# Optimization experiments

Measured on AMD Instinct MI355X. Metric: run time of the kernel, lower is better.

The kernel has to match this reference:

```python
import jax, jax.numpy as jnp
import numpy as np

N = 8192
E = 262144
IN_DIM = 128
OUT_DIM = 16


def _linear_params(key, fan_in, fan_out):
    k1, k2 = jax.random.split(key)
    bound = 1.0 / np.sqrt(fan_in)
    W = jax.random.uniform(k1, (fan_in, fan_out), jnp.float32, -bound, bound)
    b = jax.random.uniform(k2, (fan_out,), jnp.float32, -bound, bound)
    return W, b


def setup_inputs() -> dict:
    key = jax.random.key(0)
    ks = jax.random.split(key, 10)
    x = jax.random.normal(ks[0], (N, IN_DIM), jnp.float32)
    edge_index = jax.random.randint(ks[1], (2, E), 0, N, jnp.int64)
    W1, b1 = _linear_params(ks[2], IN_DIM, 128)
    W2, b2 = _linear_params(ks[3], 128, 256)
    W3, b3 = _linear_params(ks[4], 256, 64)
    Wk, bk = _linear_params(ks[5], 256, 256)
    Wq, bq = _linear_params(ks[6], 256, 256)
    Wr, br = _linear_params(ks[7], IN_DIM, 64)
    Wf, bf = _linear_params(ks[8], 64, OUT_DIM)
    ln_g = jnp.ones((64,), jnp.float32)
    ln_b = jnp.zeros((64,), jnp.float32)
    return dict(x=x, edge_index=edge_index, W1=W1, b1=b1, W2=W2, b2=b2,
                W3=W3, b3=b3, Wk=Wk, bk=bk, Wq=Wq, bq=bq, Wr=Wr, br=br,
                ln_g=ln_g, ln_b=ln_b, Wf=Wf, bf=bf)


def gcn_conv(x, W, b, row, col, n):
    # PyG GCNConv: add self-loops, symmetric normalization, aggregate src->dst
    xw = x @ W                                          # [N, F_out]
    loops = jnp.arange(n, dtype=row.dtype)
    r = jnp.concatenate([row, loops])
    c = jnp.concatenate([col, loops])
    deg = jax.ops.segment_sum(jnp.ones_like(c, jnp.float32), c, num_segments=n)
    dinv = jnp.where(deg > 0, jax.lax.rsqrt(jnp.maximum(deg, 1e-12)), 0.0)
    norm = dinv[r] * dinv[c]                            # [E+N]
    out = jax.ops.segment_sum(norm[:, None] * xw[r], c, num_segments=n)
    return out + b


def _forward(x, edge_index, W1, b1, W2, b2, W3, b3, Wk, bk, Wq, bq,
             Wr, br, ln_g, ln_b, Wf, bf):
    row, col = edge_index[0], edge_index[1]
    n = x.shape[0]
    residual = x @ Wr + br                              # [N, 64]
    h = jax.nn.leaky_relu(gcn_conv(x, W1, b1, row, col, n))   # dropout = eval no-op
    h = jax.nn.leaky_relu(gcn_conv(h, W2, b2, row, col, n))   # [N, 256]
    keys = h @ Wk + bk
    queries = h @ Wq + bq
    scores = queries @ keys.T                           # [N, N] dense, as in source
    mask = jnp.zeros((n, n), jnp.float32).at[row, col].set(1.0)
    scores = scores * mask                              # multiplicative mask (faithful)
    attn = jax.nn.softmax(scores, axis=-1)
    h = attn @ h                                        # [N, 256]
    h = jax.nn.leaky_relu(gcn_conv(h, W3, b3, row, col, n))   # [N, 64]
    z = h + residual
    mu = jnp.mean(z, axis=-1, keepdims=True)
    var = jnp.mean((z - mu) ** 2, axis=-1, keepdims=True)
    z = (z - mu) * jax.lax.rsqrt(var + 1e-5) * ln_g + ln_b
    pooled = jnp.max(z, axis=0)                         # 'max' pooling -> [64]
    return pooled @ Wf + bf                             # [OUT_DIM]


def reference(x, edge_index, W1, b1, W2, b2, W3, b3, Wk, bk, Wq, bq,
              Wr, br, ln_g, ln_b, Wf, bf):
    return _forward(x, edge_index, W1, b1, W2, b2, W3, b3, Wk, bk, Wq, bq,
                    Wr, br, ln_g, ln_b, Wf, bf)
```

## Files before the change

kernel.cpp:

```cpp
#include <hip/hip_runtime.h>
#include <hip/hip_fp16.h>
#include <cstdint>
#include <cstddef>

#define NNODES 8192
#define NEDGES 262144
#define MAXDEG 96
#define SMEM_BYTES 10496

typedef _Float16 f16x8 __attribute__((ext_vector_type(8)));
typedef _Float16 h2v   __attribute__((ext_vector_type(2)));
typedef float    f32x4 __attribute__((ext_vector_type(4)));

__device__ __forceinline__ float leaky(float v){ return v > 0.f ? v : 0.01f*v; }

__device__ __forceinline__ unsigned fmap(float f){
  unsigned u = __float_as_uint(f);
  return (u & 0x80000000u) ? ~u : (u | 0x80000000u);
}
__device__ __forceinline__ float funmap(unsigned u){
  return (u & 0x80000000u) ? __uint_as_float(u & 0x7FFFFFFFu) : __uint_as_float(~u);
}
__device__ __forceinline__ h2v as_h2(unsigned u){
  union{ unsigned x; h2v h; } c; c.x = u; return c.h;
}

struct GP {
  const float *x; const int *ei;
  const float *W1,*b1,*W2,*b2,*W3,*b3,*Wk,*bk,*Wq,*bq,*Wr,*br,*lng,*lnb,*Wf,*bfv;
  float* out;
  __half *xh,*xw1h,*h1h,*h1ah,*h2h,*qth,*gh,*hw3h;
  float *resid,*sw3;
  __half *Wqh,*Wkh,*Wqkt,*Wrt,*W1t,*W2t,*W3t;
  float *bqk,*wb,*s0p;
  int *degc,*degr,*csrc,*csrd;
  unsigned* poolpart;
};

__device__ __forceinline__ void pre_unit(const GP& p, int b, char* smem){
  int t = threadIdx.x;
  if (b < 1024){
    int base = (b*256 + t)*4;
    float4 xv = *(const float4*)(p.x + base);
    uint2 o;
    *(__half2*)&o.x = __floats2half2_rn(xv.x, xv.y);
    *(__half2*)&o.y = __floats2half2_rn(xv.z, xv.w);
    *(uint2*)(p.xh + base) = o;
  } else if (b < 1088){
    int base = ((b-1024)*256 + t)*4;
    float4 v = *(const float4*)(p.Wq + base);
    uint2 o;
    *(__half2*)&o.x = __floats2half2_rn(v.x, v.y);
    *(__half2*)&o.y = __floats2half2_rn(v.z, v.w);
    *(uint2*)(p.Wqh + base) = o;
  } else if (b < 1152){
    int base = ((b-1088)*256 + t)*4;
    float4 v = *(const float4*)(p.Wk + base);
    uint2 o;
    *(__half2*)&o.x = __floats2half2_rn(v.x, v.y);
    *(__half2*)&o.y = __floats2half2_rn(v.z, v.w);
    *(uint2*)(p.Wkh + base) = o;
  } else if (b < 1184){
    int idx = (b-1152)*256 + t;
    int nn = idx >> 7, k = idx & 127;
    p.Wrt[idx] = __float2half(p.Wr[k*64 + nn]);
  } else if (b < 1248){
    int idx = (b-1184)*256 + t;
    int nn = idx >> 7, k = idx & 127;
    p.W1t[idx] = __float2half(p.W1[k*128 + nn]);
  } else if (b < 1376){
    int idx = (b-1248)*256 + t;
    int nn = idx >> 7, k = idx & 127;
    p.W2t[idx] = __float2half(p.W2[k*256 + nn]);
  } else if (b < 1440){
    int idx = (b-1376)*256 + t;
    int nn = idx >> 8, k = idx & 255;
    p.W3t[idx] = __float2half(p.W3[k*64 + nn]);
  } else if (b < 1504){
    int idx = (b-1440)*256 + t;
    if (idx < 8192) p.degc[idx]=0; else p.degr[idx-8192]=0;
  } else if (b < 1520){
    p.poolpart[(b-1504)*256 + t] = 0u;
  } else if (b == 1520){
    if (t < 64) p.sw3[t]=0.f;
  } else {
    int c = b - 1521;
    float* ra = (float*)smem; float* rb = ra + 256; float* rc = rb + 256;
    ra[t] = p.Wk[c*256 + t] * p.bq[t];
    rb[t] = p.Wq[c*256 + t] * p.bk[t];
    if (c == 0) rc[t] = p.bq[t]*p.bk[t];
    __syncthreads();
    for (int off=128; off; off>>=1){
      if (t < off){
        ra[t] += ra[t+off];
        rb[t] += rb[t+off];
        if (c == 0) rc[t] += rc[t+off];
      }
      __syncthreads();
    }
    if (t == 0){
      p.bqk[c] = ra[0];
      p.wb[c]  = rb[0];
      if (c == 0) p.s0p[0] = rc[0];
    }
  }
}

__device__ __forceinline__ void gemm_tile(const __half* __restrict__ A,
    const __half* __restrict__ Bt, const float* __restrict__ bias,
    float* __restrict__ Cf, __half* __restrict__ Ch, float* __restrict__ csum,
    int K, int N, int act, int bx, int by,
    _Float16 (*As)[40], _Float16 (*Bs)[40], float* cs){
  int t = threadIdx.x, w = t>>6, lane = t&63;
  int m0 = bx*64, n0 = by*64;
  int quad = lane>>4, l15 = lane&15;
  int srow = t>>2, soff = (t&3)*8;
  f32x4 acc0 = {0.f,0.f,0.f,0.f}, acc1 = acc0, acc2 = acc0, acc3 = acc0;
  for (int k0 = 0; k0 < K; k0 += 32){
    *(uint4*)&As[srow][soff] = *(const uint4*)(A  + (size_t)(m0+srow)*K + k0 + soff);
    *(uint4*)&Bs[srow][soff] = *(const uint4*)(Bt + (size_t)(n0+srow)*K + k0 + soff);
    __syncthreads();
    f16x8 af = *(const f16x8*)&As[w*16 + l15][quad*8];
    f16x8 b0 = *(const f16x8*)&Bs[ 0 + l15][quad*8];
    f16x8 b1 = *(const f16x8*)&Bs[16 + l15][quad*8];
    f16x8 b2 = *(const f16x8*)&Bs[32 + l15][quad*8];
    f16x8 b3 = *(const f16x8*)&Bs[48 + l15][quad*8];
    acc0 = __builtin_amdgcn_mfma_f32_16x16x32_f16(af, b0, acc0, 0,0,0);
    acc1 = __builtin_amdgcn_mfma_f32_16x16x32_f16(af, b1, acc1, 0,0,0);
    acc2 = __builtin_amdgcn_mfma_f32_16x16x32_f16(af, b2, acc2, 0,0,0);
    acc3 = __builtin_amdgcn_mfma_f32_16x16x32_f16(af, b3, acc3, 0,0,0);
    __syncthreads();
  }
  f32x4 accs[4] = {acc0, acc1, acc2, acc3};
  if (csum){
    if (t < 64) cs[t] = 0.f;
    __syncthreads();
    #pragma unroll
    for (int nt=0; nt<4; ++nt){
      float pp = accs[nt][0]+accs[nt][1]+accs[nt][2]+accs[nt][3];
      atomicAdd(&cs[nt*16 + l15], pp);
    }
    __syncthreads();
    if (t < 64) atomicAdd(&csum[n0 + t], cs[t]);
  }
  #pragma unroll
  for (int nt=0; nt<4; ++nt){
    int col = n0 + nt*16 + l15;
    float bv = bias ? bias[col] : 0.f;
    #pragma unroll
    for (int r=0;r<4;r++){
      int row = m0 + w*16 + quad*4 + r;
      float v = accs[nt][r] + bv;
      if (act) v = leaky(v);
      if (Cf) Cf[(size_t)row*N + col] = v;
      if (Ch) Ch[(size_t)row*N + col] = __float2half(v);
    }
  }
}

template<int INS, int OUTS, int ACT>
__device__ __forceinline__ void agg128w(const __half* __restrict__ in,
    const int* __restrict__ deg, const int* __restrict__ src,
    __half* __restrict__ outp, const float* __restrict__ bias, int i){
  int lane = threadIdx.x & 63;
  int dcc = deg[i];
  float dc = rsqrtf((float)(dcc+1));
  int e0 = i*MAXDEG, e1 = e0 + dcc;
  float2 acc = make_float2(0.f, 0.f);
  for (int eb = e0; eb < e1; eb += 8){
    int m = e1 - eb; if (m > 8) m = 8;
    int r[8];
    #pragma unroll
    for (int u=0;u<8;u++) r[u] = src[(u<m) ? eb+u : eb];
    __half2 hv[8]; float sc[8];
    #pragma unroll
    for (int u=0;u<8;u++){
      hv[u] = *(const __half2*)(in + (size_t)r[u]*128 + lane*2);
      sc[u] = INS ? 1.f : rsqrtf((float)(deg[r[u]]+1));
    }
    #pragma unroll
    for (int u=0;u<8;u++){
      if (u < m){
        float2 h = __half22float2(hv[u]);
        if (INS){ acc.x += h.x; acc.y += h.y; }
        else { acc.x = fmaf(sc[u], h.x, acc.x); acc.y = fmaf(sc[u], h.y, acc.y); }
      }
    }
  }
  float2 self = __half22float2(*(const __half2*)(in + (size_t)i*128 + lane*2));
  float ss = INS ? 1.f : dc;
  float ox = dc*(ss*self.x + acc.x);
  float oy = dc*(ss*self.y + acc.y);
  if (ACT){
    ox = leaky(ox + bias[lane*2]);
    oy = leaky(oy + bias[lane*2+1]);
  }
  if (OUTS){ ox *= dc; oy *= dc; }
  *(__half2*)(outp + (size_t)i*128 + lane*2) = __floats2half2_rn(ox, oy);
}

__device__ __forceinline__ void attn_unit(const GP& p, int u){
  const int n = NNODES;
  int w = threadIdx.x>>6, lane = threadIdx.x&63;
  int i = u*4 + w;
  int fo = lane*4;
  uint2 qtu = *(const uint2*)(p.qth + (size_t)i*256 + fo);
  h2v q0 = as_h2(qtu.x), q1 = as_h2(qtu.y);
  float4 wbv = *(const float4*)(p.wb + fo);
  uint2 hiu  = *(const uint2*)(p.h2h + (size_t)i*256 + fo);
  float2 hia = __half22float2(*(__half2*)&hiu.x);
  float2 hib = __half22float2(*(__half2*)&hiu.y);
  float pv = hia.x*wbv.x + hia.y*wbv.y + hib.x*wbv.z + hib.y*wbv.w;
  #pragma unroll
  for (int mm=32; mm; mm>>=1) pv += __shfl_xor(pv, mm, 64);
  float base = pv + p.s0p[0];
  int dri = p.degr[i];
  int e0 = i*MAXDEG, e1 = e0 + dri;
  float acc = 0.f, dsum = 0.f;
  int slot = lane & 7;
  for (int eb = e0; eb < e1; eb += 8){
    int m = e1 - eb; if (m > 8) m = 8;
    int j[8];
    #pragma unroll
    for (int u8=0;u8<8;u8++) j[u8] = p.csrd[(u8<m) ? eb+u8 : eb];
    uint2 hv[8]; float gv[8];
    #pragma unroll
    for (int u8=0;u8<8;u8++){
      hv[u8] = *(const uint2*)(p.h2h + (size_t)j[u8]*256 + fo);
      gv[u8] = __half2float(p.gh[(size_t)j[u8]*64 + lane]);
    }
    float d[8];
    #pragma unroll
    for (int u8=0;u8<8;u8++)
      d[u8] = __builtin_amdgcn_fdot2(q1, as_h2(hv[u8].y),
              __builtin_amdgcn_fdot2(q0, as_h2(hv[u8].x), 0.f, false), false);
    #pragma unroll
    for (int v=0;v<8;v++) d[v] += __shfl_xor(d[v], 1, 64);
    float e0_ = (lane&1) ? d[1] : d[0];
    float e1_ = (lane&1) ? d[3] : d[2];
    float e2_ = (lane&1) ? d[5] : d[4];
    float e3_ = (lane&1) ? d[7] : d[6];
    e0_ += __shfl_xor(e0_, 2, 64);  e1_ += __shfl_xor(e1_, 2, 64);
    e2_ += __shfl_xor(e2_, 2, 64);  e3_ += __shfl_xor(e3_, 2, 64);
    float f0_ = (lane&2) ? e1_ : e0_;
    float f1_ = (lane&2) ? e3_ : e2_;
    f0_ += __shfl_xor(f0_, 4, 64);  f1_ += __shfl_xor(f1_, 4, 64);
    float g_ = (lane&4) ? f1_ : f0_;
    g_ += __shfl_xor(g_,  8, 64);
    g_ += __shfl_xor(g_, 16, 64);
    g_ += __shfl_xor(g_, 32, 64);
    float wep = __expf(g_ + base);
    float wm = (slot < m) ? wep : 0.f;
    wm += __shfl_xor(wm, 1, 64);
    wm += __shfl_xor(wm, 2, 64);
    wm += __shfl_xor(wm, 4, 64);
    dsum += wm;
    #pragma unroll
    for (int u8=0;u8<8;u8++){
      if (u8 < m){
        float wu = __shfl(wep, u8, 64);
        acc = fmaf(wu - 1.f, gv[u8], acc);
      }
    }
  }
  float inv = 1.0f / ((float)(n - dri) + dsum);
  float di = rsqrtf((float)(p.degc[i]+1));
  p.hw3h[(size_t)i*64 + lane] = __float2half(di * (p.sw3[lane] + acc) * inv);
}

__device__ __forceinline__ void zp_wave(const GP& p, int c){
  int lane = threadIdx.x & 63;
  int dcc = p.degc[c];
  float dc = rsqrtf((float)(dcc+1));
  float acc = 0.f;
  int e0 = c*MAXDEG, e1 = e0 + dcc;
  for (int eb = e0; eb < e1; eb += 8){
    int m = e1 - eb; if (m > 8) m = 8;
    int r[8];
    #pragma unroll
    for (int u=0;u<8;u++) r[u] = p.csrc[(u<m) ? eb+u : eb];
    __half hval[8];
    #pragma unroll
    for (int u=0;u<8;u++) hval[u] = p.hw3h[(size_t)r[u]*64 + lane];
    #pragma unroll
    for (int u=0;u<8;u++)
      if (u < m) acc += __half2float(hval[u]);
  }
  float self = __half2float(p.hw3h[(size_t)c*64 + lane]);
  float v = leaky(dc*(self + acc) + p.b3[lane]) + p.resid[(size_t)c*64 + lane];
  float s = v;
  #pragma unroll
  for (int mm=32; mm; mm>>=1) s += __shfl_xor(s, mm, 64);
  float mu = s * (1.0f/64.0f);
  float d = v - mu;
  float s2 = d*d;
  #pragma unroll
  for (int mm=32; mm; mm>>=1) s2 += __shfl_xor(s2, mm, 64);
  float zv = d * rsqrtf(s2*(1.0f/64.0f) + 1e-5f) * p.lng[lane] + p.lnb[lane];
  atomicMax(&p.poolpart[(c & 63)*64 + lane], fmap(zv));
}

__device__ __forceinline__ void final_unit(const GP& p, char* smem){
  int t = threadIdx.x, f = t & 63, g = t >> 6;
  unsigned (*sm)[64] = (unsigned(*)[64])smem;
  float* pool = (float*)(smem + 1024);
  unsigned mu = 0u;
  for (int b = g; b < 64; b += 4) mu = max(mu, p.poolpart[b*64 + f]);
  sm[g][f] = mu;
  __syncthreads();
  if (g == 0)
    pool[f] = funmap(max(max(sm[0][f],sm[1][f]), max(sm[2][f],sm[3][f])));
  __syncthreads();
  if (t < 16){
    float a = p.bfv[t];
    #pragma unroll
    for (int ff=0; ff<64; ++ff) a = fmaf(pool[ff], p.Wf[ff*16 + t], a);
    p.out[t] = a;
  }
}

__global__ __launch_bounds__(256) void k_pre(GP p){
  __shared__ __align__(16) char smem[SMEM_BYTES];
  pre_unit(p, blockIdx.x, smem);
}

__global__ __launch_bounds__(256) void k_sc(GP p){
  __shared__ __align__(16) char smem[SMEM_BYTES];
  _Float16 (*As)[40] = (_Float16(*)[40])smem;
  _Float16 (*Bs)[40] = (_Float16(*)[40])(smem + 5120);
  int b = blockIdx.x;
  if (b < 1024){
    int e = b*256 + threadIdx.x;
    int r = p.ei[e], c = p.ei[NEDGES+e];
    int p1 = atomicAdd(&p.degc[c],1); p.csrc[c*MAXDEG + p1] = r;
    int p2 = atomicAdd(&p.degr[r],1); p.csrd[r*MAXDEG + p2] = c;
  } else if (b < 1280){
    int bb = b - 1024;
    gemm_tile(p.xh, p.W1t, nullptr, nullptr, p.xw1h, nullptr, 128, 128, 0, bb>>1, bb&1, As, Bs, nullptr);
  } else if (b < 1296){
    int bb = b - 1280;
    gemm_tile(p.Wkh, p.Wqh, nullptr, nullptr, p.Wqkt, nullptr, 256, 256, 0, bb&3, bb>>2, As, Bs, nullptr);
  } else {
    gemm_tile(p.xh, p.Wrt, p.br, p.resid, nullptr, nullptr, 128, 64, 0, b-1296, 0, As, Bs, nullptr);
  }
}

__global__ __launch_bounds__(256) void k_agg0(GP p){
  int i = blockIdx.x*4 + (threadIdx.x>>6);
  agg128w<0,1,1>(p.xw1h, p.degc, p.csrc, p.h1h, p.b1, i);
}
__global__ __launch_bounds__(256) void k_agg1(GP p){
  int i = blockIdx.x*4 + (threadIdx.x>>6);
  agg128w<1,0,0>(p.h1h, p.degc, p.csrc, p.h1ah, nullptr, i);
}

__global__ __launch_bounds__(256) void k_gemm2(GP p){
  __shared__ __align__(16) char smem[SMEM_BYTES];
  _Float16 (*As)[40] = (_Float16(*)[40])smem;
  _Float16 (*Bs)[40] = (_Float16(*)[40])(smem + 5120);
  int b = blockIdx.x;
  gemm_tile(p.h1ah, p.W2t, p.b2, nullptr, p.h2h, nullptr, 128, 256, 1, b>>2, b&3, As, Bs, nullptr);
}

__global__ __launch_bounds__(256) void k_mix2(GP p){
  __shared__ __align__(16) char smem[SMEM_BYTES];
  _Float16 (*As)[40] = (_Float16(*)[40])smem;
  _Float16 (*Bs)[40] = (_Float16(*)[40])(smem + 5120);
  float* cs = (float*)(smem + 10240);
  int b = blockIdx.x;
  if (b < 128) gemm_tile(p.h2h, p.W3t, nullptr, nullptr, p.gh, p.sw3, 256, 64, 0, b, 0, As, Bs, cs);
  else {
    int bb = b - 128;
    gemm_tile(p.h2h, p.Wqkt, p.bqk, nullptr, p.qth, nullptr, 256, 256, 0, bb>>2, bb&3, As, Bs, cs);
  }
}

__global__ __launch_bounds__(256) void k_attn(GP p){ attn_unit(p, blockIdx.x); }

__global__ __launch_bounds__(256) void k_zp(GP p){
  int c = blockIdx.x*4 + (threadIdx.x>>6);
  zp_wave(p, c);
}

__global__ __launch_bounds__(256) void k_final(GP p){
  __shared__ __align__(16) char smem[SMEM_BYTES];
  final_unit(p, smem);
}

extern "C" void kernel_launch(void* const* d_in, const int* in_sizes, int n_in,
                              void* d_out, int out_size, void* d_ws, size_t ws_size,
                              hipStream_t stream){
  const int n = NNODES, E = NEDGES;
  char* ws = (char*)d_ws; size_t off = 0;
  auto alloc = [&](size_t bytes)->void*{
    void* pp = ws + off; off += (bytes + 255) & ~(size_t)255; return pp;
  };
  GP p;
  p.x   = (const float*)d_in[0];
  p.ei  = (const int*)d_in[1];
  p.W1  = (const float*)d_in[2];  p.b1 = (const float*)d_in[3];
  p.W2  = (const float*)d_in[4];  p.b2 = (const float*)d_in[5];
  p.W3  = (const float*)d_in[6];  p.b3 = (const float*)d_in[7];
  p.Wk  = (const float*)d_in[8];  p.bk = (const float*)d_in[9];
  p.Wq  = (const float*)d_in[10]; p.bq = (const float*)d_in[11];
  p.Wr  = (const float*)d_in[12]; p.br = (const float*)d_in[13];
  p.lng = (const float*)d_in[14]; p.lnb = (const float*)d_in[15];
  p.Wf  = (const float*)d_in[16]; p.bfv = (const float*)d_in[17];
  p.out = (float*)d_out;

  p.xh   = (__half*)alloc((size_t)n*128*2);
  p.xw1h = (__half*)alloc((size_t)n*128*2);
  p.h1h  = (__half*)alloc((size_t)n*128*2);
  p.h1ah = (__half*)alloc((size_t)n*128*2);
  p.h2h  = (__half*)alloc((size_t)n*256*2);
  p.qth  = (__half*)alloc((size_t)n*256*2);
  p.gh   = (__half*)alloc((size_t)n*64*2);
  p.hw3h = (__half*)alloc((size_t)n*64*2);
  p.resid= (float*)alloc((size_t)n*64*4);
  p.sw3  = (float*)alloc(64*4);
  p.Wqh  = (__half*)alloc(256*256*2);
  p.Wkh  = (__half*)alloc(256*256*2);
  p.Wqkt = (__half*)alloc(256*256*2);
  p.Wrt  = (__half*)alloc(128*64*2);
  p.W1t  = (__half*)alloc(128*128*2);
  p.W2t  = (__half*)alloc(128*256*2);
  p.W3t  = (__half*)alloc(256*64*2);
  p.bqk  = (float*)alloc(256*4);
  p.wb   = (float*)alloc(256*4);
  p.s0p  = (float*)alloc(4);
  p.degc = (int*)alloc((size_t)n*4);
  p.degr = (int*)alloc((size_t)n*4);
  p.csrc = (int*)alloc((size_t)n*MAXDEG*4);
  p.csrd = (int*)alloc((size_t)n*MAXDEG*4);
  p.poolpart = (unsigned*)alloc(64*64*4);

  k_pre  <<<dim3(1777), 256, 0, stream>>>(p);
  k_sc   <<<dim3(1424), 256, 0, stream>>>(p);
  k_agg0 <<<dim3(n/4),  256, 0, stream>>>(p);
  k_agg1 <<<dim3(n/4),  256, 0, stream>>>(p);
  k_gemm2<<<dim3(512),  256, 0, stream>>>(p);
  k_mix2 <<<dim3(640),  256, 0, stream>>>(p);
  k_attn <<<dim3(n/4),  256, 0, stream>>>(p);
  k_zp   <<<dim3(n/4),  256, 0, stream>>>(p);
  k_final<<<dim3(1),    256, 0, stream>>>(p);
}
```

Measured before the change: 213.4 us.

## Fuse fp32-to-fp16 conversion into GEMM tile loads and merge prep kernels

Removes the separate pre-conversion pass that wrote fp16 copies of x, Wq, Wk, Wr and W1. The GEMMs now read fp32 directly and convert while staging into shared memory, with a strided transposed read for W1/Wr. The remaining prep work (W2/W3 transpose, pool and sw3 zeroing, bias folding) is merged into the scatter/GEMM kernel. A tiny zeroing kernel clears degc/degr, which are now placed next to each other so one int4 store pass covers both. This cuts one full-size launch and the x fp16 round trip, at the cost of scalar strided B loads and per-element converts inside the GEMM loads.

```diff
diff --git a/kernel.cpp b/kernel.cpp
--- a/kernel.cpp
+++ b/kernel.cpp
@@ -29,82 +29,13 @@
   const float *x; const int *ei;
   const float *W1,*b1,*W2,*b2,*W3,*b3,*Wk,*bk,*Wq,*bq,*Wr,*br,*lng,*lnb,*Wf,*bfv;
   float* out;
-  __half *xh,*xw1h,*h1h,*h1ah,*h2h,*qth,*gh,*hw3h;
+  __half *xw1h,*h1h,*h1ah,*h2h,*qth,*gh,*hw3h;
   float *resid,*sw3;
-  __half *Wqh,*Wkh,*Wqkt,*Wrt,*W1t,*W2t,*W3t;
+  __half *Wqkt,*W2t,*W3t;
   float *bqk,*wb,*s0p;
   int *degc,*degr,*csrc,*csrd;
   unsigned* poolpart;
 };
-
-__device__ __forceinline__ void pre_unit(const GP& p, int b, char* smem){
-  int t = threadIdx.x;
-  if (b < 1024){
-    int base = (b*256 + t)*4;
-    float4 xv = *(const float4*)(p.x + base);
-    uint2 o;
-    *(__half2*)&o.x = __floats2half2_rn(xv.x, xv.y);
-    *(__half2*)&o.y = __floats2half2_rn(xv.z, xv.w);
-    *(uint2*)(p.xh + base) = o;
-  } else if (b < 1088){
-    int base = ((b-1024)*256 + t)*4;
-    float4 v = *(const float4*)(p.Wq + base);
-    uint2 o;
-    *(__half2*)&o.x = __floats2half2_rn(v.x, v.y);
-    *(__half2*)&o.y = __floats2half2_rn(v.z, v.w);
-    *(uint2*)(p.Wqh + base) = o;
-  } else if (b < 1152){
-    int base = ((b-1088)*256 + t)*4;
-    float4 v = *(const float4*)(p.Wk + base);
-    uint2 o;
-    *(__half2*)&o.x = __floats2half2_rn(v.x, v.y);
-    *(__half2*)&o.y = __floats2half2_rn(v.z, v.w);
-    *(uint2*)(p.Wkh + base) = o;
-  } else if (b < 1184){
-    int idx = (b-1152)*256 + t;
-    int nn = idx >> 7, k = idx & 127;
-    p.Wrt[idx] = __float2half(p.Wr[k*64 + nn]);
-  } else if (b < 1248){
-    int idx = (b-1184)*256 + t;
-    int nn = idx >> 7, k = idx & 127;
-    p.W1t[idx] = __float2half(p.W1[k*128 + nn]);
-  } else if (b < 1376){
-    int idx = (b-1248)*256 + t;
-    int nn = idx >> 7, k = idx & 127;
-    p.W2t[idx] = __float2half(p.W2[k*256 + nn]);
-  } else if (b < 1440){
-    int idx = (b-1376)*256 + t;
-    int nn = idx >> 8, k = idx & 255;
-    p.W3t[idx] = __float2half(p.W3[k*64 + nn]);
-  } else if (b < 1504){
-    int idx = (b-1440)*256 + t;
-    if (idx < 8192) p.degc[idx]=0; else p.degr[idx-8192]=0;
-  } else if (b < 1520){
-    p.poolpart[(b-1504)*256 + t] = 0u;
-  } else if (b == 1520){
-    if (t < 64) p.sw3[t]=0.f;
-  } else {
-    int c = b - 1521;
-    float* ra = (float*)smem; float* rb = ra + 256; float* rc = rb + 256;
-    ra[t] = p.Wk[c*256 + t] * p.bq[t];
-    rb[t] = p.Wq[c*256 + t] * p.bk[t];
-    if (c == 0) rc[t] = p.bq[t]*p.bk[t];
-    __syncthreads();
-    for (int off=128; off; off>>=1){
-      if (t < off){
-        ra[t] += ra[t+off];
-        rb[t] += rb[t+off];
-        if (c == 0) rc[t] += rc[t+off];
-      }
-      __syncthreads();
-    }
-    if (t == 0){
-      p.bqk[c] = ra[0];
-      p.wb[c]  = rb[0];
-      if (c == 0) p.s0p[0] = rc[0];
-    }
-  }
-}
 
 __device__ __forceinline__ void gemm_tile(const __half* __restrict__ A,
     const __half* __restrict__ Bt, const float* __restrict__ bias,
@@ -152,6 +83,61 @@
       int row = m0 + w*16 + quad*4 + r;
       float v = accs[nt][r] + bv;
       if (act) v = leaky(v);
+      if (Cf) Cf[(size_t)row*N + col] = v;
+      if (Ch) Ch[(size_t)row*N + col] = __float2half(v);
+    }
+  }
+}
+
+template<int TRANSB>
+__device__ __forceinline__ void gemm_f32(const float* __restrict__ A,
+    const float* __restrict__ B, const float* __restrict__ bias,
+    float* __restrict__ Cf, __half* __restrict__ Ch,
+    int K, int N, int bx, int by,
+    _Float16 (*As)[40], _Float16 (*Bs)[40]){
+  int t = threadIdx.x, w = t>>6, lane = t&63;
+  int m0 = bx*64, n0 = by*64;
+  int quad = lane>>4, l15 = lane&15;
+  int srow = t>>2, soff = (t&3)*8;
+  f32x4 acc0 = {0.f,0.f,0.f,0.f}, acc1 = acc0, acc2 = acc0, acc3 = acc0;
+  for (int k0 = 0; k0 < K; k0 += 32){
+    float4 a0 = *(const float4*)(A + (size_t)(m0+srow)*K + k0 + soff);
+    float4 a1 = *(const float4*)(A + (size_t)(m0+srow)*K + k0 + soff + 4);
+    _Float16* ad = &As[srow][soff];
+    ad[0]=(_Float16)a0.x; ad[1]=(_Float16)a0.y; ad[2]=(_Float16)a0.z; ad[3]=(_Float16)a0.w;
+    ad[4]=(_Float16)a1.x; ad[5]=(_Float16)a1.y; ad[6]=(_Float16)a1.z; ad[7]=(_Float16)a1.w;
+    _Float16* bd = &Bs[srow][soff];
+    if (TRANSB){
+      #pragma unroll
+      for (int u=0;u<8;u++)
+        bd[u] = (_Float16)B[(size_t)(k0+soff+u)*N + n0+srow];
+    } else {
+      float4 b0 = *(const float4*)(B + (size_t)(n0+srow)*K + k0 + soff);
+      float4 b1 = *(const float4*)(B + (size_t)(n0+srow)*K + k0 + soff + 4);
+      bd[0]=(_Float16)b0.x; bd[1]=(_Float16)b0.y; bd[2]=(_Float16)b0.z; bd[3]=(_Float16)b0.w;
+      bd[4]=(_Float16)b1.x; bd[5]=(_Float16)b1.y; bd[6]=(_Float16)b1.z; bd[7]=(_Float16)b1.w;
+    }
+    __syncthreads();
+    f16x8 af = *(const f16x8*)&As[w*16 + l15][quad*8];
+    f16x8 b0 = *(const f16x8*)&Bs[ 0 + l15][quad*8];
+    f16x8 b1 = *(const f16x8*)&Bs[16 + l15][quad*8];
+    f16x8 b2 = *(const f16x8*)&Bs[32 + l15][quad*8];
+    f16x8 b3 = *(const f16x8*)&Bs[48 + l15][quad*8];
+    acc0 = __builtin_amdgcn_mfma_f32_16x16x32_f16(af, b0, acc0, 0,0,0);
+    acc1 = __builtin_amdgcn_mfma_f32_16x16x32_f16(af, b1, acc1, 0,0,0);
+    acc2 = __builtin_amdgcn_mfma_f32_16x16x32_f16(af, b2, acc2, 0,0,0);
+    acc3 = __builtin_amdgcn_mfma_f32_16x16x32_f16(af, b3, acc3, 0,0,0);
+    __syncthreads();
+  }
+  f32x4 accs[4] = {acc0, acc1, acc2, acc3};
+  #pragma unroll
+  for (int nt=0; nt<4; ++nt){
+    int col = n0 + nt*16 + l15;
+    float bv = bias ? bias[col] : 0.f;
+    #pragma unroll
+    for (int r=0;r<4;r++){
+      int row = m0 + w*16 + quad*4 + r;
+      float v = accs[nt][r] + bv;
       if (Cf) Cf[(size_t)row*N + col] = v;
       if (Ch) Ch[(size_t)row*N + col] = __float2half(v);
     }
@@ -319,29 +305,62 @@
   }
 }
 
+__global__ __launch_bounds__(256) void k_z(GP p){
+  int idx = blockIdx.x*256 + threadIdx.x;
+  int4 z = {0,0,0,0};
+  ((int4*)p.degc)[idx] = z;
+}
+
 __global__ __launch_bounds__(256) void k_pre(GP p){
-  __shared__ __align__(16) char smem[SMEM_BYTES];
-  pre_unit(p, blockIdx.x, smem);
-}
-
-__global__ __launch_bounds__(256) void k_sc(GP p){
   __shared__ __align__(16) char smem[SMEM_BYTES];
   _Float16 (*As)[40] = (_Float16(*)[40])smem;
   _Float16 (*Bs)[40] = (_Float16(*)[40])(smem + 5120);
-  int b = blockIdx.x;
+  int b = blockIdx.x, t = threadIdx.x;
   if (b < 1024){
-    int e = b*256 + threadIdx.x;
+    int e = b*256 + t;
     int r = p.ei[e], c = p.ei[NEDGES+e];
     int p1 = atomicAdd(&p.degc[c],1); p.csrc[c*MAXDEG + p1] = r;
     int p2 = atomicAdd(&p.degr[r],1); p.csrd[r*MAXDEG + p2] = c;
   } else if (b < 1280){
     int bb = b - 1024;
-    gemm_tile(p.xh, p.W1t, nullptr, nullptr, p.xw1h, nullptr, 128, 128, 0, bb>>1, bb&1, As, Bs, nullptr);
+    gemm_f32<1>(p.x, p.W1, nullptr, nullptr, p.xw1h, 128, 128, bb>>1, bb&1, As, Bs);
   } else if (b < 1296){
     int bb = b - 1280;
-    gemm_tile(p.Wkh, p.Wqh, nullptr, nullptr, p.Wqkt, nullptr, 256, 256, 0, bb&3, bb>>2, As, Bs, nullptr);
+    gemm_f32<0>(p.Wk, p.Wq, nullptr, nullptr, p.Wqkt, 256, 256, bb&3, bb>>2, As, Bs);
+  } else if (b < 1424){
+    gemm_f32<1>(p.x, p.Wr, p.br, p.resid, nullptr, 128, 64, b-1296, 0, As, Bs);
+  } else if (b < 1552){
+    int idx = (b-1424)*256 + t;
+    int nn = idx >> 7, k = idx & 127;
+    p.W2t[idx] = __float2half(p.W2[k*256 + nn]);
+  } else if (b < 1616){
+    int idx = (b-1552)*256 + t;
+    int nn = idx >> 8, k = idx & 255;
+    p.W3t[idx] = __float2half(p.W3[k*64 + nn]);
+  } else if (b < 1632){
+    p.poolpart[(b-1616)*256 + t] = 0u;
+  } else if (b == 1632){
+    if (t < 64) p.sw3[t] = 0.f;
   } else {
-    gemm_tile(p.xh, p.Wrt, p.br, p.resid, nullptr, nullptr, 128, 64, 0, b-1296, 0, As, Bs, nullptr);
+    int c = b - 1633;
+    float* ra = (float*)smem; float* rb = ra + 256; float* rc = rb + 256;
+    ra[t] = p.Wk[c*256 + t] * p.bq[t];
+    rb[t] = p.Wq[c*256 + t] * p.bk[t];
+    if (c == 0) rc[t] = p.bq[t]*p.bk[t];
+    __syncthreads();
+    for (int off=128; off; off>>=1){
+      if (t < off){
+        ra[t] += ra[t+off];
+        rb[t] += rb[t+off];
+        if (c == 0) rc[t] += rc[t+off];
+      }
+      __syncthreads();
+    }
+    if (t == 0){
+      p.bqk[c] = ra[0];
+      p.wb[c]  = rb[0];
+      if (c == 0) p.s0p[0] = rc[0];
+    }
   }
 }
 
@@ -408,7 +427,8 @@
   p.Wf  = (const float*)d_in[16]; p.bfv = (const float*)d_in[17];
   p.out = (float*)d_out;
 
-  p.xh   = (__half*)alloc((size_t)n*128*2);
+  p.degc = (int*)alloc((size_t)n*4);
+  p.degr = (int*)alloc((size_t)n*4);
   p.xw1h = (__half*)alloc((size_t)n*128*2);
   p.h1h  = (__half*)alloc((size_t)n*128*2);
   p.h1ah = (__half*)alloc((size_t)n*128*2);
@@ -418,24 +438,18 @@
   p.hw3h = (__half*)alloc((size_t)n*64*2);
   p.resid= (float*)alloc((size_t)n*64*4);
   p.sw3  = (float*)alloc(64*4);
-  p.Wqh  = (__half*)alloc(256*256*2);
-  p.Wkh  = (__half*)alloc(256*256*2);
   p.Wqkt = (__half*)alloc(256*256*2);
-  p.Wrt  = (__half*)alloc(128*64*2);
-  p.W1t  = (__half*)alloc(128*128*2);
   p.W2t  = (__half*)alloc(128*256*2);
   p.W3t  = (__half*)alloc(256*64*2);
   p.bqk  = (float*)alloc(256*4);
   p.wb   = (float*)alloc(256*4);
   p.s0p  = (float*)alloc(4);
-  p.degc = (int*)alloc((size_t)n*4);
-  p.degr = (int*)alloc((size_t)n*4);
   p.csrc = (int*)alloc((size_t)n*MAXDEG*4);
   p.csrd = (int*)alloc((size_t)n*MAXDEG*4);
   p.poolpart = (unsigned*)alloc(64*64*4);
 
-  k_pre  <<<dim3(1777), 256, 0, stream>>>(p);
-  k_sc   <<<dim3(1424), 256, 0, stream>>>(p);
+  k_z    <<<dim3(16),   256, 0, stream>>>(p);
+  k_pre  <<<dim3(1889), 256, 0, stream>>>(p);
   k_agg0 <<<dim3(n/4),  256, 0, stream>>>(p);
   k_agg1 <<<dim3(n/4),  256, 0, stream>>>(p);
   k_gemm2<<<dim3(512),  256, 0, stream>>>(p);
```

Result: faster. 204.9 us (-4.0%).
